# Kernel tuning notes

Measured on AMD Instinct MI355X. Metric: run time of the kernel, lower is better.

Reference implementation:

```python
import jax, jax.numpy as jnp
import numpy as np

T, C, H, E, TOPK = 8192, 1024, 4096, 8, 2
ALPHA = 0.01


def setup_inputs() -> dict:
    key = jax.random.key(0)
    ks = jax.random.split(key, 10)
    std = 0.01
    return {
        "x": jax.random.normal(ks[0], (T, C), dtype=jnp.float32),
        "gate_w": jax.random.normal(ks[1], (E, C), dtype=jnp.float32) * std,  # nn.init.normal_(std=0.01)
        "wg": jax.random.normal(ks[2], (E, C, H), dtype=jnp.float32) * 0.02,
        "wu": jax.random.normal(ks[3], (E, C, H), dtype=jnp.float32) * 0.02,
        "wd": jax.random.normal(ks[4], (E, H, C), dtype=jnp.float32) * 0.02,
        "swg": jax.random.normal(ks[5], (C, H), dtype=jnp.float32) * 0.02,
        "swu": jax.random.normal(ks[6], (C, H), dtype=jnp.float32) * 0.02,
        "swd": jax.random.normal(ks[7], (H, C), dtype=jnp.float32) * 0.02,
        "shared_scale": jnp.ones((1,), dtype=jnp.float32) * 0.5,
    }


def _swiglu(h, g, u, d):
    # SwiGLU FFN: W_down( silu(W_gate x) * W_up x )
    return (jax.nn.silu(h @ g) * (h @ u)) @ d


def reference(x, gate_w, wg, wu, wd, swg, swu, swd, shared_scale):
    # ---- gate (top-k softmax routing) ----
    logits = x @ gate_w.T                       # [T, E]
    scores = jax.nn.softmax(logits, axis=-1)    # [T, E]
    topk_w, topk_idx = jax.lax.top_k(scores, TOPK)
    topk_w = topk_w / jnp.sum(topk_w, axis=-1, keepdims=True)

    # per-token combine weight for each expert: sum_k w_k * [idx_k == e]  -> [T, E]
    comb = jnp.zeros((x.shape[0], E), dtype=x.dtype)
    comb = comb.at[jnp.arange(x.shape[0])[:, None], topk_idx].add(topk_w)

    # ---- routed experts (dispatch-FFN-combine, expressed as masked dense combine) ----
    y = jnp.zeros_like(x)
    for e in range(E):  # fixed small expert count
        y = y + comb[:, e:e + 1] * _swiglu(x, wg[e], wu[e], wd[e])

    # ---- shared expert ----
    y = y + shared_scale * _swiglu(x, swg, swu, swd)

    # ---- load-balancing aux loss (training mode) ----
    onehot = jax.nn.one_hot(topk_idx.reshape(-1), E, dtype=x.dtype)  # [T*K, E]
    ce = onehot.mean(axis=0)
    fi = ce * E
    Pi = scores.mean(axis=0)
    aux_loss = jnp.sum(Pi * fi) * ALPHA
    return y, aux_loss
```

## Files before the change

### kernel.cpp

```cpp
#include <hip/hip_runtime.h>
#include <hip/hip_bf16.h>
#include <stdint.h>

#define T_TOK 8192
#define CDIM  1024
#define HDIM  4096
#define NEXP  8
#define TOPK_ 2
#define GT_MAX 72
#define UT_MAX 104
#define GROWS_MAX (GT_MAX * 256)

typedef __attribute__((ext_vector_type(8))) short short8;
typedef __attribute__((ext_vector_type(4))) float f32x4;

__device__ __forceinline__ void gload16(const short* g, short* l) {
  __builtin_amdgcn_global_load_lds(
      (const __attribute__((address_space(1))) unsigned int*)(g),
      (__attribute__((address_space(3))) unsigned int*)(l), 16, 0, 0);
}

__global__ __launch_bounds__(256) void gate_kernel(
    const float* __restrict__ x, const float* __restrict__ gw,
    int* __restrict__ tokinfo, float* __restrict__ tokw,
    int* __restrict__ bcnt, float* __restrict__ spart)
{
  const int wid = threadIdx.x >> 6, lane = threadIdx.x & 63;
  const int t = blockIdx.x * 4 + wid;
  float acc[NEXP];
#pragma unroll
  for (int e = 0; e < NEXP; ++e) acc[e] = 0.f;
  const float4* xr = (const float4*)x + (size_t)t * (CDIM / 4);
  const float4* gw4 = (const float4*)gw;
#pragma unroll
  for (int i = 0; i < CDIM / 256; ++i) {
    const float4 xv = xr[lane + 64 * i];
#pragma unroll
    for (int e = 0; e < NEXP; ++e) {
      const float4 gv = gw4[e * (CDIM / 4) + lane + 64 * i];
      acc[e] += xv.x * gv.x + xv.y * gv.y + xv.z * gv.z + xv.w * gv.w;
    }
  }
#pragma unroll
  for (int off = 32; off > 0; off >>= 1) {
#pragma unroll
    for (int e = 0; e < NEXP; ++e) acc[e] += __shfl_xor(acc[e], off);
  }
  float mx = acc[0];
#pragma unroll
  for (int e = 1; e < NEXP; ++e) mx = fmaxf(mx, acc[e]);
  float p[NEXP]; float s = 0.f;
#pragma unroll
  for (int e = 0; e < NEXP; ++e) { p[e] = __expf(acc[e] - mx); s += p[e]; }
  const float inv = 1.f / s;
#pragma unroll
  for (int e = 0; e < NEXP; ++e) p[e] *= inv;
  float v0 = p[0]; int i0 = 0;
#pragma unroll
  for (int e = 1; e < NEXP; ++e) if (p[e] > v0) { v0 = p[e]; i0 = e; }
  float v1 = -1.f; int i1 = 0;
#pragma unroll
  for (int e = 0; e < NEXP; ++e) if (e != i0 && p[e] > v1) { v1 = p[e]; i1 = e; }

  __shared__ float sp[4][NEXP];
  __shared__ int   se[4][2];
  __shared__ float swt[4][2];
  if (lane == 0) {
#pragma unroll
    for (int e = 0; e < NEXP; ++e) sp[wid][e] = p[e];
    const float wn = 1.f / (v0 + v1);
    se[wid][0] = i0; se[wid][1] = i1;
    swt[wid][0] = v0 * wn; swt[wid][1] = v1 * wn;
  }
  __syncthreads();
  if (threadIdx.x == 0) {
    int cnt[NEXP];
#pragma unroll
    for (int e = 0; e < NEXP; ++e) cnt[e] = 0;
#pragma unroll
    for (int tt = 0; tt < 4; ++tt) {
      const int e0 = se[tt][0], e1 = se[tt][1];
      const int r0 = cnt[e0]++; const int r1 = cnt[e1]++;
      tokinfo[blockIdx.x * 4 + tt] = e0 | (e1 << 3) | (r0 << 6) | (r1 << 10);
      ((float2*)tokw)[blockIdx.x * 4 + tt] = make_float2(swt[tt][0], swt[tt][1]);
    }
#pragma unroll
    for (int e = 0; e < NEXP; ++e) bcnt[blockIdx.x * NEXP + e] = cnt[e];
  }
  if (threadIdx.x < NEXP)
    spart[blockIdx.x * NEXP + threadIdx.x] =
        sp[0][threadIdx.x] + sp[1][threadIdx.x] + sp[2][threadIdx.x] + sp[3][threadIdx.x];
}

__global__ __launch_bounds__(512) void scan_kernel(
    const int* __restrict__ bcnt, int* __restrict__ boff, int* __restrict__ ecnt,
    const float* __restrict__ spart, float* __restrict__ aux_out,
    int* __restrict__ pad_off, int* __restrict__ tile_map, int* __restrict__ ntiles)
{
  const int w = threadIdx.x >> 6, l = threadIdx.x & 63;
  int run = 0;
#pragma unroll 4
  for (int c = 0; c < (T_TOK / 4) / 64; ++c) {
    const int b = c * 64 + l;
    const int v = bcnt[b * NEXP + w];
    int sc = v;
#pragma unroll
    for (int off = 1; off < 64; off <<= 1) {
      const int t = __shfl_up(sc, off);
      if (l >= off) sc += t;
    }
    boff[b * NEXP + w] = run + sc - v;
    run += __shfl(sc, 63);
  }
  if (l == 0) ecnt[w] = run;
  float fs = 0.f;
  for (int c = 0; c < (T_TOK / 4) / 64; ++c) fs += spart[(c * 64 + l) * NEXP + w];
#pragma unroll
  for (int off = 32; off > 0; off >>= 1) fs += __shfl_xor(fs, off);
  __shared__ float pis[NEXP];
  __shared__ int cs[NEXP];
  if (l == 0) { pis[w] = fs; cs[w] = run; }
  __syncthreads();
  if (threadIdx.x == 0) {
    float aux = 0.f;
#pragma unroll
    for (int e = 0; e < NEXP; ++e) {
      const float Pi = pis[e] / (float)T_TOK;
      const float ce = (float)cs[e] / (float)(T_TOK * TOPK_);
      aux += Pi * ce * (float)NEXP;
    }
    aux_out[0] = aux * 0.01f;
    ecnt[8] = T_TOK;
    int acc = 0, nt = 0;
    for (int e = 0; e < NEXP; ++e) {
      pad_off[e] = acc;
      const int te = (cs[e] + 255) >> 8;
      for (int t = 0; t < te; ++t) { tile_map[nt] = e | ((t * 256) << 4); ++nt; }
      acc += te * 256;
    }
    ntiles[0] = nt;
    for (int t = 0; t < T_TOK / 256; ++t) { tile_map[nt] = 8 | ((t * 256) << 4); ++nt; }
    ntiles[1] = nt;
  }
}

__global__ __launch_bounds__(256) void scatter_kernel(
    const int* __restrict__ tokinfo, const float* __restrict__ tokw,
    const int* __restrict__ boff, const int* __restrict__ pad_off,
    int* __restrict__ grows, float* __restrict__ gww)
{
  const int t = blockIdx.x * 256 + threadIdx.x;
  const int info = tokinfo[t];
  const int e0 = info & 7, e1 = (info >> 3) & 7;
  const int r0 = (info >> 6) & 15, r1 = (info >> 10) & 15;
  const int b = t >> 2;
  const float2 wv = ((const float2*)tokw)[t];
  const int g0 = pad_off[e0] + boff[b * NEXP + e0] + r0;
  grows[g0] = t; gww[g0] = wv.x;
  const int g1 = pad_off[e1] + boff[b * NEXP + e1] + r1;
  grows[g1] = t; gww[g1] = wv.y;
}

__global__ __launch_bounds__(256) void cvt_x_kernel(const float* __restrict__ x,
                                                    __hip_bfloat16* __restrict__ xb)
{
  const int i = blockIdx.x * 256 + threadIdx.x;
  const float4 v = ((const float4*)x)[i];
  union { __hip_bfloat16 h[4]; uint2 u; } o;
  o.h[0] = __float2bfloat16(v.x); o.h[1] = __float2bfloat16(v.y);
  o.h[2] = __float2bfloat16(v.z); o.h[3] = __float2bfloat16(v.w);
  ((uint2*)xb)[i] = o.u;
}

struct TD { const float* src; __hip_bfloat16* dst; int N; int nsh; int M; };
struct TB { TD d[27]; };
__global__ __launch_bounds__(256) void tbatch_kernel(TB tb)
{
  const int m = blockIdx.x >> 12;
  const int t = blockIdx.x & 4095;
  const TD td = tb.d[m];
  const int n0 = (t & ((1 << td.nsh) - 1)) << 5;
  const int m0 = (t >> td.nsh) << 5;
  __shared__ float tile[32][33];
  const int tx = threadIdx.x & 31, ty = threadIdx.x >> 5;
#pragma unroll
  for (int i = 0; i < 4; ++i)
    tile[ty + 8 * i][tx] = td.src[(size_t)(m0 + ty + 8 * i) * td.N + n0 + tx];
  __syncthreads();
#pragma unroll
  for (int i = 0; i < 4; ++i)
    td.dst[(size_t)(n0 + ty + 8 * i) * td.M + m0 + tx] = __float2bfloat16(tile[tx][ty + 8 * i]);
}

template <int OP>
__global__ __launch_bounds__(512, 2) void gemm_pipe_kernel(
    const __hip_bfloat16* __restrict__ Abase,
    const __hip_bfloat16* __restrict__ B0mat,
    const __hip_bfloat16* __restrict__ B1mat,
    __hip_bfloat16* __restrict__ midout,
    float* __restrict__ y,
    const int* __restrict__ rowlist, const float* __restrict__ roww,
    const int* __restrict__ ecnt, const int* __restrict__ tile_map,
    const int* __restrict__ ntiles, const float* __restrict__ ssc,
    int mode, int tile_base)
{
  constexpr int K = (OP == 1) ? CDIM : HDIM;
  constexpr int NT = 32;
  __shared__ __align__(16) short lds[65536];

  int ti = blockIdx.y + tile_base;
  if (mode == 2) ti += ntiles[0];
  const int hi = (mode == 1) ? ntiles[0] : ntiles[1];
  if (ti >= hi) return;
  const int tm = tile_map[ti];
  const int e = tm & 15, rb = tm >> 4;
  const int rows_valid = ecnt[e] - rb;
  const int gbmid = (int)blockIdx.y * 256;
  const int glist = ti * 256;
  const int kbase = (OP == 2) ? (int)blockIdx.z * 1024 : 0;

  const int t = threadIdx.x, l = t & 63, w = t >> 6;
  const int sr = t >> 2;
  const int csrc = (t & 3) ^ ((t >> 3) & 3);
  const int n0 = blockIdx.x * ((OP == 1) ? 128 : 256);

  const short *pA0, *pA1, *pB0, *pB1;
  if (OP == 1) {
    int r0g, r1g;
    if (e == 8) { r0g = rb + sr; r1g = rb + 128 + sr; }
    else {
      const int c0 = sr < rows_valid ? sr : rows_valid - 1;
      const int c1 = (128 + sr) < rows_valid ? (128 + sr) : rows_valid - 1;
      r0g = rowlist[glist + c0]; r1g = rowlist[glist + c1];
    }
    pA0 = (const short*)Abase + (size_t)r0g * K + csrc * 8;
    pA1 = (const short*)Abase + (size_t)r1g * K + csrc * 8;
    const int br0 = sr, br1 = 128 + sr;
    const int s0 = (br0 >> 4) & 1, s1 = (br1 >> 4) & 1;
    const int h0 = n0 + (br0 >> 5) * 16 + (br0 & 15);
    const int h1 = n0 + (br1 >> 5) * 16 + (br1 & 15);
    pB0 = (const short*)(s0 ? B1mat : B0mat) + (size_t)e * CDIM * HDIM + (size_t)h0 * K + csrc * 8;
    pB1 = (const short*)(s1 ? B1mat : B0mat) + (size_t)e * CDIM * HDIM + (size_t)h1 * K + csrc * 8;
  } else {
    pA0 = (const short*)Abase + (size_t)(gbmid + sr) * K + kbase + csrc * 8;
    pA1 = (const short*)Abase + (size_t)(gbmid + 128 + sr) * K + kbase + csrc * 8;
    const short* bb = (const short*)B0mat + (size_t)e * CDIM * HDIM;
    pB0 = bb + (size_t)(n0 + sr) * K + kbase + csrc * 8;
    pB1 = bb + (size_t)(n0 + 128 + sr) * K + kbase + csrc * 8;
  }
  short* dstA = lds + w * 512;
  short* dstB = lds + 32768 + w * 512;

  const int wr = w >> 2, wc = w & 3;
  const int cswz = (l >> 1) & 3;
  const int chunk = (((l >> 4) ^ cswz) << 3);
  const int afb = wr * 4096 + (l & 15) * 32 + chunk;
  const int bfb = 32768 + (wc >> 1) * 4096 + ((wc & 1) * 64 + (l & 15)) * 32 + chunk;

  f32x4 acc[8][4];
#pragma unroll
  for (int i = 0; i < 8; ++i)
#pragma unroll
    for (int j = 0; j < 4; ++j) acc[i][j] = (f32x4){0.f, 0.f, 0.f, 0.f};

#define STAGE_A(q) { const int s8_ = ((q) & 3) * 8192; \
    gload16(pA0 + (q) * 32, dstA + s8_); \
    gload16(pA1 + (q) * 32, dstA + s8_ + 4096); }
#define STAGE_B(q) { const int s8_ = ((q) & 3) * 8192; \
    gload16(pB0 + (q) * 32, dstB + s8_); \
    gload16(pB1 + (q) * 32, dstB + s8_ + 4096); }

  STAGE_A(0) STAGE_B(0) STAGE_A(1) STAGE_B(1)

  short8 af[8], bf[4];
  for (int q = 0; q < NT; ++q) {
    const int s8 = (q & 3) * 8192;
    if (q == NT - 1) {
      asm volatile("s_waitcnt vmcnt(0)\n\ts_barrier" ::: "memory");
    } else {
      asm volatile("s_waitcnt vmcnt(4)\n\ts_barrier" ::: "memory");
    }
    __builtin_amdgcn_sched_barrier(0);
    if (q + 2 < NT) STAGE_A(q + 2)
#pragma unroll
    for (int mi = 0; mi < 4; ++mi) af[mi] = *(const short8*)(lds + s8 + afb + mi * 512);
#pragma unroll
    for (int ni = 0; ni < 4; ++ni) bf[ni] = *(const short8*)(lds + s8 + bfb + ni * 512);
#pragma unroll
    for (int mi = 4; mi < 8; ++mi) af[mi] = *(const short8*)(lds + s8 + afb + mi * 512);
    __builtin_amdgcn_s_setprio(1);
#pragma unroll
    for (int mi = 0; mi < 4; ++mi)
#pragma unroll
      for (int ni = 0; ni < 4; ++ni)
        acc[mi][ni] = __builtin_amdgcn_mfma_f32_16x16x32_bf16(af[mi], bf[ni], acc[mi][ni], 0, 0, 0);
    __builtin_amdgcn_s_setprio(0);
    if (q + 2 < NT) STAGE_B(q + 2)
    __builtin_amdgcn_s_setprio(1);
#pragma unroll
    for (int mi = 4; mi < 8; ++mi)
#pragma unroll
      for (int ni = 0; ni < 4; ++ni)
        acc[mi][ni] = __builtin_amdgcn_mfma_f32_16x16x32_bf16(af[mi], bf[ni], acc[mi][ni], 0, 0, 0);
    __builtin_amdgcn_s_setprio(0);
  }
#undef STAGE_A
#undef STAGE_B

  const int rl = (l >> 4) * 4, cl = l & 15;
  if (OP == 1) {
#pragma unroll
    for (int mi = 0; mi < 8; ++mi) {
#pragma unroll
      for (int j = 0; j < 4; ++j) {
        const int rlocal = wr * 128 + mi * 16 + rl + j;
        if (rlocal < rows_valid) {
          __hip_bfloat16* mp = midout + (size_t)(gbmid + rlocal) * HDIM;
#pragma unroll
          for (int jj = 0; jj < 2; ++jj) {
            const float g = acc[mi][jj * 2][j], u = acc[mi][jj * 2 + 1][j];
            const float sv = g / (1.f + __expf(-g));
            mp[n0 + (wc * 2 + jj) * 16 + cl] = __float2bfloat16(sv * u);
          }
        }
      }
    }
  } else {
    const float ss = ssc[0];
#pragma unroll
    for (int mi = 0; mi < 8; ++mi) {
#pragma unroll
      for (int j = 0; j < 4; ++j) {
        const int rlocal = wr * 128 + mi * 16 + rl + j;
        if (rlocal < rows_valid) {
          int tok; float wgt;
          if (e == 8) { tok = rb + rlocal; wgt = ss; }
          else { tok = rowlist[glist + rlocal]; wgt = roww[glist + rlocal]; }
          float* yp = y + (size_t)tok * CDIM + n0 + wc * 64 + cl;
#pragma unroll
          for (int ni = 0; ni < 4; ++ni)
            unsafeAtomicAdd(yp + ni * 16, wgt * acc[mi][ni][j]);
        }
      }
    }
  }
}

extern "C" void kernel_launch(void* const* d_in, const int* in_sizes, int n_in,
                              void* d_out, int out_size, void* d_ws, size_t ws_size,
                              hipStream_t stream)
{
  const float* x   = (const float*)d_in[0];
  const float* gw  = (const float*)d_in[1];
  const float* wg  = (const float*)d_in[2];
  const float* wu  = (const float*)d_in[3];
  const float* wd  = (const float*)d_in[4];
  const float* swg = (const float*)d_in[5];
  const float* swu = (const float*)d_in[6];
  const float* swd = (const float*)d_in[7];
  const float* ssc = (const float*)d_in[8];
  float* y = (float*)d_out;

  auto al = [](size_t v) { return (v + 255) & ~(size_t)255; };
  char* ws = (char*)d_ws;
  size_t off = 0;
  __hip_bfloat16* xb = (__hip_bfloat16*)(ws + off); off += al((size_t)T_TOK * CDIM * 2);
  int*   tokinfo = (int*)(ws + off);   off += al((size_t)T_TOK * 4);
  float* tokw    = (float*)(ws + off); off += al((size_t)T_TOK * 8);
  int*   bcnt    = (int*)(ws + off);   off += al((size_t)(T_TOK / 4) * NEXP * 4);
  int*   boffb   = (int*)(ws + off);   off += al((size_t)(T_TOK / 4) * NEXP * 4);
  float* spart   = (float*)(ws + off); off += al((size_t)(T_TOK / 4) * NEXP * 4);
  int*   ecnt    = (int*)(ws + off);   off += 256;
  int*   pad_off = (int*)(ws + off);   off += 256;
  int*   ntiles  = (int*)(ws + off);   off += 256;
  int*   tile_map= (int*)(ws + off);   off += al((size_t)UT_MAX * 4);
  int*   grows   = (int*)(ws + off);   off += al((size_t)GROWS_MAX * 4);
  float* gww     = (float*)(ws + off); off += al((size_t)GROWS_MAX * 4);

  const size_t WMAT = (size_t)CDIM * HDIM;
  __hip_bfloat16* wg9 = (__hip_bfloat16*)(ws + off); off += 9 * WMAT * 2;
  __hip_bfloat16* wu9 = (__hip_bfloat16*)(ws + off); off += 9 * WMAT * 2;
  __hip_bfloat16* wd9 = (__hip_bfloat16*)(ws + off); off += 9 * WMAT * 2;
  __hip_bfloat16* mid = (__hip_bfloat16*)(ws + off);
  const size_t mid_avail = (ws_size > off) ? (ws_size - off) : 0;
  const size_t TILE_B = (size_t)256 * HDIM * 2;

  hipMemsetAsync(y, 0, (size_t)(T_TOK * CDIM + 1) * sizeof(float), stream);
  gate_kernel<<<T_TOK / 4, 256, 0, stream>>>(x, gw, tokinfo, tokw, bcnt, spart);
  scan_kernel<<<1, 512, 0, stream>>>(bcnt, boffb, ecnt, spart, y + (size_t)T_TOK * CDIM,
                                     pad_off, tile_map, ntiles);
  scatter_kernel<<<T_TOK / 256, 256, 0, stream>>>(tokinfo, tokw, boffb, pad_off, grows, gww);
  cvt_x_kernel<<<T_TOK * CDIM / 4 / 256, 256, 0, stream>>>(x, xb);

  TB tb;
  for (int e = 0; e < 8; ++e) {
    tb.d[e]      = TD{wg + e * WMAT, wg9 + e * WMAT, HDIM, 7, CDIM};
    tb.d[8 + e]  = TD{wu + e * WMAT, wu9 + e * WMAT, HDIM, 7, CDIM};
    tb.d[16 + e] = TD{wd + e * WMAT, wd9 + e * WMAT, CDIM, 5, HDIM};
  }
  tb.d[24] = TD{swg, wg9 + 8 * WMAT, HDIM, 7, CDIM};
  tb.d[25] = TD{swu, wu9 + 8 * WMAT, HDIM, 7, CDIM};
  tb.d[26] = TD{swd, wd9 + 8 * WMAT, CDIM, 5, HDIM};
  tbatch_kernel<<<27 * 4096, 256, 0, stream>>>(tb);

  if (mid_avail >= (size_t)UT_MAX * TILE_B) {
    gemm_pipe_kernel<1><<<dim3(HDIM / 128, UT_MAX), 512, 0, stream>>>(
        xb, wg9, wu9, mid, nullptr, grows, gww, ecnt, tile_map, ntiles, ssc, 0, 0);
    gemm_pipe_kernel<2><<<dim3(CDIM / 256, UT_MAX, 4), 512, 0, stream>>>(
        mid, wd9, nullptr, nullptr, y, grows, gww, ecnt, tile_map, ntiles, ssc, 0, 0);
  } else if (mid_avail >= (size_t)GT_MAX * TILE_B) {
    gemm_pipe_kernel<1><<<dim3(HDIM / 128, GT_MAX), 512, 0, stream>>>(
        xb, wg9, wu9, mid, nullptr, grows, gww, ecnt, tile_map, ntiles, ssc, 1, 0);
    gemm_pipe_kernel<2><<<dim3(CDIM / 256, GT_MAX, 4), 512, 0, stream>>>(
        mid, wd9, nullptr, nullptr, y, grows, gww, ecnt, tile_map, ntiles, ssc, 1, 0);
    gemm_pipe_kernel<1><<<dim3(HDIM / 128, 32), 512, 0, stream>>>(
        xb, wg9, wu9, mid, nullptr, grows, gww, ecnt, tile_map, ntiles, ssc, 2, 0);
    gemm_pipe_kernel<2><<<dim3(CDIM / 256, 32, 4), 512, 0, stream>>>(
        mid, wd9, nullptr, nullptr, y, grows, gww, ecnt, tile_map, ntiles, ssc, 2, 0);
  } else {
    int CH = (int)(mid_avail / TILE_B);
    if (CH < 1) CH = 1;
    for (int c0 = 0; c0 < GT_MAX; c0 += CH) {
      const int g = (GT_MAX - c0) < CH ? (GT_MAX - c0) : CH;
      gemm_pipe_kernel<1><<<dim3(HDIM / 128, g), 512, 0, stream>>>(
          xb, wg9, wu9, mid, nullptr, grows, gww, ecnt, tile_map, ntiles, ssc, 1, c0);
      gemm_pipe_kernel<2><<<dim3(CDIM / 256, g, 4), 512, 0, stream>>>(
          mid, wd9, nullptr, nullptr, y, grows, gww, ecnt, tile_map, ntiles, ssc, 1, c0);
    }
    for (int c0 = 0; c0 < 32; c0 += CH) {
      const int g = (32 - c0) < CH ? (32 - c0) : CH;
      gemm_pipe_kernel<1><<<dim3(HDIM / 128, g), 512, 0, stream>>>(
          xb, wg9, wu9, mid, nullptr, grows, gww, ecnt, tile_map, ntiles, ssc, 2, c0);
      gemm_pipe_kernel<2><<<dim3(CDIM / 256, g, 4), 512, 0, stream>>>(
          mid, wd9, nullptr, nullptr, y, grows, gww, ecnt, tile_map, ntiles, ssc, 2, c0);
    }
  }
}
```

Before: 1.040 ms.

## Replace split-K atomic down-projection with full-K GEMM and deterministic combine kernel

Splits the templated GEMM into separate up and down kernels. The down-projection GEMM now covers the full K=4096 with 128-wide N tiles and no split-K. When enough workspace is available, it writes per-row fp32 partials to a buffer, and a new combine kernel gathers each token's two routed rows plus its shared-expert row, weighting and summing them. This removes the y memset and the fp32 atomic adds, at the cost of an extra fp32 write and read of about 100 tiles×256×1024. Full-K tiles also lower parallelism in the down GEMM.

```diff
diff --git a/kernel.cpp b/kernel.cpp
--- a/kernel.cpp
+++ b/kernel.cpp
@@ -147,7 +147,7 @@
 __global__ __launch_bounds__(256) void scatter_kernel(
     const int* __restrict__ tokinfo, const float* __restrict__ tokw,
     const int* __restrict__ boff, const int* __restrict__ pad_off,
-    int* __restrict__ grows, float* __restrict__ gww)
+    int* __restrict__ grows, float* __restrict__ gww, int2* __restrict__ tokpos)
 {
   const int t = blockIdx.x * 256 + threadIdx.x;
   const int info = tokinfo[t];
@@ -159,6 +159,7 @@
   grows[g0] = t; gww[g0] = wv.x;
   const int g1 = pad_off[e1] + boff[b * NEXP + e1] + r1;
   grows[g1] = t; gww[g1] = wv.y;
+  tokpos[t] = make_int2(g0, g1);
 }
 
 __global__ __launch_bounds__(256) void cvt_x_kernel(const float* __restrict__ x,
@@ -192,19 +193,15 @@
     td.dst[(size_t)(n0 + ty + 8 * i) * td.M + m0 + tx] = __float2bfloat16(tile[tx][ty + 8 * i]);
 }
 
-template <int OP>
-__global__ __launch_bounds__(512, 2) void gemm_pipe_kernel(
+__global__ __launch_bounds__(512, 2) void gemm1_pipe_kernel(
     const __hip_bfloat16* __restrict__ Abase,
-    const __hip_bfloat16* __restrict__ B0mat,
-    const __hip_bfloat16* __restrict__ B1mat,
+    const __hip_bfloat16* __restrict__ B0mat, const __hip_bfloat16* __restrict__ B1mat,
     __hip_bfloat16* __restrict__ midout,
-    float* __restrict__ y,
-    const int* __restrict__ rowlist, const float* __restrict__ roww,
-    const int* __restrict__ ecnt, const int* __restrict__ tile_map,
-    const int* __restrict__ ntiles, const float* __restrict__ ssc,
+    const int* __restrict__ rowlist, const int* __restrict__ ecnt,
+    const int* __restrict__ tile_map, const int* __restrict__ ntiles,
     int mode, int tile_base)
 {
-  constexpr int K = (OP == 1) ? CDIM : HDIM;
+  constexpr int K = CDIM;
   constexpr int NT = 32;
   __shared__ __align__(16) short lds[65536];
 
@@ -217,43 +214,33 @@
   const int rows_valid = ecnt[e] - rb;
   const int gbmid = (int)blockIdx.y * 256;
   const int glist = ti * 256;
-  const int kbase = (OP == 2) ? (int)blockIdx.z * 1024 : 0;
 
   const int t = threadIdx.x, l = t & 63, w = t >> 6;
   const int sr = t >> 2;
   const int csrc = (t & 3) ^ ((t >> 3) & 3);
-  const int n0 = blockIdx.x * ((OP == 1) ? 128 : 256);
-
-  const short *pA0, *pA1, *pB0, *pB1;
-  if (OP == 1) {
-    int r0g, r1g;
-    if (e == 8) { r0g = rb + sr; r1g = rb + 128 + sr; }
-    else {
-      const int c0 = sr < rows_valid ? sr : rows_valid - 1;
-      const int c1 = (128 + sr) < rows_valid ? (128 + sr) : rows_valid - 1;
-      r0g = rowlist[glist + c0]; r1g = rowlist[glist + c1];
-    }
-    pA0 = (const short*)Abase + (size_t)r0g * K + csrc * 8;
-    pA1 = (const short*)Abase + (size_t)r1g * K + csrc * 8;
-    const int br0 = sr, br1 = 128 + sr;
-    const int s0 = (br0 >> 4) & 1, s1 = (br1 >> 4) & 1;
-    const int h0 = n0 + (br0 >> 5) * 16 + (br0 & 15);
-    const int h1 = n0 + (br1 >> 5) * 16 + (br1 & 15);
-    pB0 = (const short*)(s0 ? B1mat : B0mat) + (size_t)e * CDIM * HDIM + (size_t)h0 * K + csrc * 8;
-    pB1 = (const short*)(s1 ? B1mat : B0mat) + (size_t)e * CDIM * HDIM + (size_t)h1 * K + csrc * 8;
-  } else {
-    pA0 = (const short*)Abase + (size_t)(gbmid + sr) * K + kbase + csrc * 8;
-    pA1 = (const short*)Abase + (size_t)(gbmid + 128 + sr) * K + kbase + csrc * 8;
-    const short* bb = (const short*)B0mat + (size_t)e * CDIM * HDIM;
-    pB0 = bb + (size_t)(n0 + sr) * K + kbase + csrc * 8;
-    pB1 = bb + (size_t)(n0 + 128 + sr) * K + kbase + csrc * 8;
-  }
+  const int n0 = blockIdx.x * 128;
+
+  int r0g, r1g;
+  if (e == 8) { r0g = rb + sr; r1g = rb + 128 + sr; }
+  else {
+    const int c0 = sr < rows_valid ? sr : rows_valid - 1;
+    const int c1 = (128 + sr) < rows_valid ? (128 + sr) : rows_valid - 1;
+    r0g = rowlist[glist + c0]; r1g = rowlist[glist + c1];
+  }
+  const short* pA0 = (const short*)Abase + (size_t)r0g * K + csrc * 8;
+  const short* pA1 = (const short*)Abase + (size_t)r1g * K + csrc * 8;
+  const int br0 = sr, br1 = 128 + sr;
+  const int s0 = (br0 >> 4) & 1, s1 = (br1 >> 4) & 1;
+  const int h0 = n0 + (br0 >> 5) * 16 + (br0 & 15);
+  const int h1 = n0 + (br1 >> 5) * 16 + (br1 & 15);
+  const short* pB0 = (const short*)(s0 ? B1mat : B0mat) + (size_t)e * CDIM * HDIM + (size_t)h0 * K + csrc * 8;
+  const short* pB1 = (const short*)(s1 ? B1mat : B0mat) + (size_t)e * CDIM * HDIM + (size_t)h1 * K + csrc * 8;
+
   short* dstA = lds + w * 512;
   short* dstB = lds + 32768 + w * 512;
 
   const int wr = w >> 2, wc = w & 3;
-  const int cswz = (l >> 1) & 3;
-  const int chunk = (((l >> 4) ^ cswz) << 3);
+  const int chunk = (((l >> 4) ^ ((l >> 1) & 3)) << 3);
   const int afb = wr * 4096 + (l & 15) * 32 + chunk;
   const int bfb = 32768 + (wc >> 1) * 4096 + ((wc & 1) * 64 + (l & 15)) * 32 + chunk;
 
@@ -308,20 +295,112 @@
 #undef STAGE_B
 
   const int rl = (l >> 4) * 4, cl = l & 15;
-  if (OP == 1) {
+#pragma unroll
+  for (int mi = 0; mi < 8; ++mi) {
+#pragma unroll
+    for (int j = 0; j < 4; ++j) {
+      const int rlocal = wr * 128 + mi * 16 + rl + j;
+      if (rlocal < rows_valid) {
+        __hip_bfloat16* mp = midout + (size_t)(gbmid + rlocal) * HDIM;
+#pragma unroll
+        for (int jj = 0; jj < 2; ++jj) {
+          const float g = acc[mi][jj * 2][j], u = acc[mi][jj * 2 + 1][j];
+          const float sv = g / (1.f + __expf(-g));
+          mp[n0 + (wc * 2 + jj) * 16 + cl] = __float2bfloat16(sv * u);
+        }
+      }
+    }
+  }
+}
+
+template <int OST>
+__global__ __launch_bounds__(512, 1) void gemm2_pipe_kernel(
+    const __hip_bfloat16* __restrict__ mid, const __hip_bfloat16* __restrict__ wd9,
+    float* __restrict__ mid2, float* __restrict__ y,
+    const int* __restrict__ rowlist, const float* __restrict__ roww,
+    const int* __restrict__ ecnt, const int* __restrict__ tile_map,
+    const int* __restrict__ ntiles, const float* __restrict__ ssc,
+    int mode, int tile_base)
+{
+  constexpr int K = HDIM;
+  constexpr int NT = K / 32;
+  __shared__ __align__(16) short lds[49152];
+
+  int ti = blockIdx.y + tile_base;
+  if (mode == 2) ti += ntiles[0];
+  const int hi = (mode == 1) ? ntiles[0] : ntiles[1];
+  if (ti >= hi) return;
+  const int tm = tile_map[ti];
+  const int e = tm & 15, rb = tm >> 4;
+  const int rows_valid = ecnt[e] - rb;
+  const int gbmid = (int)blockIdx.y * 256;
+  const int glist = ti * 256;
+
+  const int t = threadIdx.x, l = t & 63, w = t >> 6;
+  const int sr = t >> 2;
+  const int csrc = (t & 3) ^ ((t >> 3) & 3);
+  const int n0 = blockIdx.x * 128;
+
+  const short* pA0 = (const short*)mid + (size_t)(gbmid + sr) * K + csrc * 8;
+  const short* pA1 = pA0 + (size_t)128 * K;
+  const short* pB0 = (const short*)wd9 + (size_t)e * CDIM * HDIM + (size_t)(n0 + sr) * K + csrc * 8;
+
+  short* dA = lds + w * 512;
+  short* dB = lds + 32768 + w * 512;
+
+  const int wr = w >> 2, wc = w & 3;
+  const int chunk = (((l >> 4) ^ ((l >> 1) & 3)) << 3);
+  const int afb = wr * 4096 + (l & 15) * 32 + chunk;
+  const int bfb = 32768 + (wc * 32 + (l & 15)) * 32 + chunk;
+
+  f32x4 acc[8][2];
+#pragma unroll
+  for (int i = 0; i < 8; ++i) { acc[i][0] = (f32x4){0.f,0.f,0.f,0.f}; acc[i][1] = (f32x4){0.f,0.f,0.f,0.f}; }
+
+#define S_A(q) { const int o_ = ((q) & 3) * 8192; \
+    gload16(pA0 + (size_t)(q) * 32, dA + o_); \
+    gload16(pA1 + (size_t)(q) * 32, dA + o_ + 4096); }
+#define S_B(q) { const int o_ = ((q) & 3) * 4096; \
+    gload16(pB0 + (size_t)(q) * 32, dB + o_); }
+
+  S_A(0) S_B(0) S_A(1) S_B(1)
+
+  short8 af[8], bf[2];
+  for (int q = 0; q < NT; ++q) {
+    const int sA = (q & 3) * 8192, sB = (q & 3) * 4096;
+    if (q == NT - 1) {
+      asm volatile("s_waitcnt vmcnt(0)\n\ts_barrier" ::: "memory");
+    } else {
+      asm volatile("s_waitcnt vmcnt(3)\n\ts_barrier" ::: "memory");
+    }
+    __builtin_amdgcn_sched_barrier(0);
+    if (q + 2 < NT) { S_A(q + 2) S_B(q + 2) }
+#pragma unroll
+    for (int mi = 0; mi < 8; ++mi) af[mi] = *(const short8*)(lds + sA + afb + mi * 512);
+    bf[0] = *(const short8*)(lds + sB + bfb);
+    bf[1] = *(const short8*)(lds + sB + bfb + 512);
+    __builtin_amdgcn_s_setprio(1);
+#pragma unroll
+    for (int mi = 0; mi < 8; ++mi) {
+      acc[mi][0] = __builtin_amdgcn_mfma_f32_16x16x32_bf16(af[mi], bf[0], acc[mi][0], 0, 0, 0);
+      acc[mi][1] = __builtin_amdgcn_mfma_f32_16x16x32_bf16(af[mi], bf[1], acc[mi][1], 0, 0, 0);
+    }
+    __builtin_amdgcn_s_setprio(0);
+  }
+#undef S_A
+#undef S_B
+
+  const int rl = (l >> 4) * 4, cl = l & 15;
+  if (OST) {
 #pragma unroll
     for (int mi = 0; mi < 8; ++mi) {
 #pragma unroll
       for (int j = 0; j < 4; ++j) {
         const int rlocal = wr * 128 + mi * 16 + rl + j;
         if (rlocal < rows_valid) {
-          __hip_bfloat16* mp = midout + (size_t)(gbmid + rlocal) * HDIM;
-#pragma unroll
-          for (int jj = 0; jj < 2; ++jj) {
-            const float g = acc[mi][jj * 2][j], u = acc[mi][jj * 2 + 1][j];
-            const float sv = g / (1.f + __expf(-g));
-            mp[n0 + (wc * 2 + jj) * 16 + cl] = __float2bfloat16(sv * u);
-          }
+          float* mp = mid2 + (size_t)(glist + rlocal) * CDIM + n0 + wc * 32 + cl;
+          mp[0]  = acc[mi][0][j];
+          mp[16] = acc[mi][1][j];
         }
       }
     }
@@ -336,14 +415,35 @@
           int tok; float wgt;
           if (e == 8) { tok = rb + rlocal; wgt = ss; }
           else { tok = rowlist[glist + rlocal]; wgt = roww[glist + rlocal]; }
-          float* yp = y + (size_t)tok * CDIM + n0 + wc * 64 + cl;
-#pragma unroll
-          for (int ni = 0; ni < 4; ++ni)
-            unsafeAtomicAdd(yp + ni * 16, wgt * acc[mi][ni][j]);
+          float* yp = y + (size_t)tok * CDIM + n0 + wc * 32 + cl;
+          unsafeAtomicAdd(yp,      wgt * acc[mi][0][j]);
+          unsafeAtomicAdd(yp + 16, wgt * acc[mi][1][j]);
         }
       }
     }
   }
+}
+
+__global__ __launch_bounds__(256) void combine_kernel(
+    const float* __restrict__ mid2, const int* __restrict__ ntiles,
+    const int2* __restrict__ tokpos, const float* __restrict__ tokw,
+    const float* __restrict__ ssc, float* __restrict__ y)
+{
+  const int t = blockIdx.x;
+  const int c = threadIdx.x * 4;
+  const int dbase = ntiles[0] * 256;
+  const int2 gp = tokpos[t];
+  const float2 wv = ((const float2*)tokw)[t];
+  const float ss = ssc[0];
+  const float4 d = *(const float4*)(mid2 + (size_t)(dbase + t) * CDIM + c);
+  const float4 a = *(const float4*)(mid2 + (size_t)gp.x * CDIM + c);
+  const float4 b = *(const float4*)(mid2 + (size_t)gp.y * CDIM + c);
+  float4 r;
+  r.x = ss * d.x + wv.x * a.x + wv.y * b.x;
+  r.y = ss * d.y + wv.x * a.y + wv.y * b.y;
+  r.z = ss * d.z + wv.x * a.z + wv.y * b.z;
+  r.w = ss * d.w + wv.x * a.w + wv.y * b.w;
+  *(float4*)(y + (size_t)t * CDIM + c) = r;
 }
 
 extern "C" void kernel_launch(void* const* d_in, const int* in_sizes, int n_in,
@@ -367,6 +467,7 @@
   __hip_bfloat16* xb = (__hip_bfloat16*)(ws + off); off += al((size_t)T_TOK * CDIM * 2);
   int*   tokinfo = (int*)(ws + off);   off += al((size_t)T_TOK * 4);
   float* tokw    = (float*)(ws + off); off += al((size_t)T_TOK * 8);
+  int2*  tokpos  = (int2*)(ws + off);  off += al((size_t)T_TOK * 8);
   int*   bcnt    = (int*)(ws + off);   off += al((size_t)(T_TOK / 4) * NEXP * 4);
   int*   boffb   = (int*)(ws + off);   off += al((size_t)(T_TOK / 4) * NEXP * 4);
   float* spart   = (float*)(ws + off); off += al((size_t)(T_TOK / 4) * NEXP * 4);
@@ -384,12 +485,14 @@
   __hip_bfloat16* mid = (__hip_bfloat16*)(ws + off);
   const size_t mid_avail = (ws_size > off) ? (ws_size - off) : 0;
   const size_t TILE_B = (size_t)256 * HDIM * 2;
-
-  hipMemsetAsync(y, 0, (size_t)(T_TOK * CDIM + 1) * sizeof(float), stream);
+  const size_t MIDB   = (size_t)UT_MAX * TILE_B;
+  const size_t MID2B  = (size_t)UT_MAX * 256 * CDIM * 4;
+
   gate_kernel<<<T_TOK / 4, 256, 0, stream>>>(x, gw, tokinfo, tokw, bcnt, spart);
   scan_kernel<<<1, 512, 0, stream>>>(bcnt, boffb, ecnt, spart, y + (size_t)T_TOK * CDIM,
                                      pad_off, tile_map, ntiles);
-  scatter_kernel<<<T_TOK / 256, 256, 0, stream>>>(tokinfo, tokw, boffb, pad_off, grows, gww);
+  scatter_kernel<<<T_TOK / 256, 256, 0, stream>>>(tokinfo, tokw, boffb, pad_off,
+                                                  grows, gww, tokpos);
   cvt_x_kernel<<<T_TOK * CDIM / 4 / 256, 256, 0, stream>>>(x, xb);
 
   TB tb;
@@ -403,36 +506,36 @@
   tb.d[26] = TD{swd, wd9 + 8 * WMAT, CDIM, 5, HDIM};
   tbatch_kernel<<<27 * 4096, 256, 0, stream>>>(tb);
 
-  if (mid_avail >= (size_t)UT_MAX * TILE_B) {
-    gemm_pipe_kernel<1><<<dim3(HDIM / 128, UT_MAX), 512, 0, stream>>>(
-        xb, wg9, wu9, mid, nullptr, grows, gww, ecnt, tile_map, ntiles, ssc, 0, 0);
-    gemm_pipe_kernel<2><<<dim3(CDIM / 256, UT_MAX, 4), 512, 0, stream>>>(
-        mid, wd9, nullptr, nullptr, y, grows, gww, ecnt, tile_map, ntiles, ssc, 0, 0);
-  } else if (mid_avail >= (size_t)GT_MAX * TILE_B) {
-    gemm_pipe_kernel<1><<<dim3(HDIM / 128, GT_MAX), 512, 0, stream>>>(
-        xb, wg9, wu9, mid, nullptr, grows, gww, ecnt, tile_map, ntiles, ssc, 1, 0);
-    gemm_pipe_kernel<2><<<dim3(CDIM / 256, GT_MAX, 4), 512, 0, stream>>>(
-        mid, wd9, nullptr, nullptr, y, grows, gww, ecnt, tile_map, ntiles, ssc, 1, 0);
-    gemm_pipe_kernel<1><<<dim3(HDIM / 128, 32), 512, 0, stream>>>(
-        xb, wg9, wu9, mid, nullptr, grows, gww, ecnt, tile_map, ntiles, ssc, 2, 0);
-    gemm_pipe_kernel<2><<<dim3(CDIM / 256, 32, 4), 512, 0, stream>>>(
-        mid, wd9, nullptr, nullptr, y, grows, gww, ecnt, tile_map, ntiles, ssc, 2, 0);
+  if (mid_avail >= MIDB + MID2B) {
+    float* mid2 = (float*)((char*)mid + MIDB);
+    gemm1_pipe_kernel<<<dim3(HDIM / 128, UT_MAX), 512, 0, stream>>>(
+        xb, wg9, wu9, mid, grows, ecnt, tile_map, ntiles, 0, 0);
+    gemm2_pipe_kernel<1><<<dim3(CDIM / 128, UT_MAX), 512, 0, stream>>>(
+        mid, wd9, mid2, nullptr, grows, gww, ecnt, tile_map, ntiles, ssc, 0, 0);
+    combine_kernel<<<T_TOK, 256, 0, stream>>>(mid2, ntiles, tokpos, tokw, ssc, y);
+  } else if (mid_avail >= MIDB) {
+    hipMemsetAsync(y, 0, (size_t)T_TOK * CDIM * sizeof(float), stream);
+    gemm1_pipe_kernel<<<dim3(HDIM / 128, UT_MAX), 512, 0, stream>>>(
+        xb, wg9, wu9, mid, grows, ecnt, tile_map, ntiles, 0, 0);
+    gemm2_pipe_kernel<0><<<dim3(CDIM / 128, UT_MAX), 512, 0, stream>>>(
+        mid, wd9, nullptr, y, grows, gww, ecnt, tile_map, ntiles, ssc, 0, 0);
   } else {
+    hipMemsetAsync(y, 0, (size_t)T_TOK * CDIM * sizeof(float), stream);
     int CH = (int)(mid_avail / TILE_B);
     if (CH < 1) CH = 1;
     for (int c0 = 0; c0 < GT_MAX; c0 += CH) {
       const int g = (GT_MAX - c0) < CH ? (GT_MAX - c0) : CH;
-      gemm_pipe_kernel<1><<<dim3(HDIM / 128, g), 512, 0, stream>>>(
-          xb, wg9, wu9, mid, nullptr, grows, gww, ecnt, tile_map, ntiles, ssc, 1, c0);
-      gemm_pipe_kernel<2><<<dim3(CDIM / 256, g, 4), 512, 0, stream>>>(
-          mid, wd9, nullptr, nullptr, y, grows, gww, ecnt, tile_map, ntiles, ssc, 1, c0);
+      gemm1_pipe_kernel<<<dim3(HDIM / 128, g), 512, 0, stream>>>(
+          xb, wg9, wu9, mid, grows, ecnt, tile_map, ntiles, 1, c0);
+      gemm2_pipe_kernel<0><<<dim3(CDIM / 128, g), 512, 0, stream>>>(
+          mid, wd9, nullptr, y, grows, gww, ecnt, tile_map, ntiles, ssc, 1, c0);
     }
     for (int c0 = 0; c0 < 32; c0 += CH) {
       const int g = (32 - c0) < CH ? (32 - c0) : CH;
-      gemm_pipe_kernel<1><<<dim3(HDIM / 128, g), 512, 0, stream>>>(
-          xb, wg9, wu9, mid, nullptr, grows, gww, ecnt, tile_map, ntiles, ssc, 2, c0);
-      gemm_pipe_kernel<2><<<dim3(CDIM / 256, g, 4), 512, 0, stream>>>(
-          mid, wd9, nullptr, nullptr, y, grows, gww, ecnt, tile_map, ntiles, ssc, 2, c0);
-    }
-  }
-}
+      gemm1_pipe_kernel<<<dim3(HDIM / 128, g), 512, 0, stream>>>(
+          xb, wg9, wu9, mid, grows, ecnt, tile_map, ntiles, 2, c0);
+      gemm2_pipe_kernel<0><<<dim3(CDIM / 128, g), 512, 0, stream>>>(
+          mid, wd9, nullptr, y, grows, gww, ecnt, tile_map, ntiles, ssc, 2, c0);
+    }
+  }
+}
```

Measured after the change: 1.006 ms. -3.3%, faster.
